# Kernel tuning notes

Hardware: AMD Instinct MI355X
Metric: run time of the kernel (lower is better)

The kernel has to match this reference:

```python
import jax, jax.numpy as jnp
import numpy as np

B = 256      # batch
ZD = 128     # z_dim
HIN = 128    # H_inputs
H = 512      # hidden
HT = 32      # H_t
N = 16384    # num nodes
RW = 16      # rw_len
TEMP = 1.0
P_DROP = 0.2
EPS_C = 0.1  # constraints epsilon


def setup_inputs() -> dict:
    key = jax.random.key(0)
    ks = jax.random.split(key, 20)
    def w(k, shape, fan):
        return (jax.random.normal(k, shape, jnp.float32) / np.float32(np.sqrt(fan)))
    z = lambda n: jnp.zeros((n,), jnp.float32)
    u = jax.random.uniform(ks[14], (RW, B, N), jnp.float32)
    return {
        "latent": jax.random.normal(ks[0], (B, ZD + 1), jnp.float32),
        "inputs0": jnp.zeros((B, HIN), jnp.float32),
        "Wc": w(ks[1], (ZD, ZD + 1), ZD + 1), "bc": z(ZD),
        "Ws": w(ks[2], (H, ZD), ZD), "bs": z(H),
        "Wh": w(ks[3], (H, H), H), "bh": z(H),
        "Wcc": w(ks[4], (H, H), H), "bcc": z(H),
        "W_ih": w(ks[5], (4 * H, HIN), HIN), "b_ih": z(4 * H),
        "W_hh": w(ks[6], (4 * H, H), H), "b_hh": z(4 * H),
        "W_up": w(ks[7], (N, H), H), "b_up": z(N),
        "W_down": w(ks[8], (HIN, N), N),
        "Wt_down": w(ks[9], (HT, H), H), "bt_down": z(HT),
        "Wt_pred": w(ks[10], (1, HT), HT),
        "Wt_up": w(ks[11], (HT, 1), 1), "bt_up": z(HT),
        "W_vt": w(ks[12], (HIN, HIN + HT), HIN + HT),
        "W_prob": w(ks[13], (1, HIN), HIN),
        # pre-sampled Gumbel noise per step (torch.rand -> gumbel)
        "gumbel": -jnp.log(-jnp.log(u + 1e-20) + 1e-20),
        # uniforms for dropout masks in TimeDecoder (forced train mode)
        "drop_u": jax.random.uniform(ks[15], (RW, B, HT), jnp.float32),
    }


def reference(latent, inputs0, Wc, bc, Ws, bs, Wh, bh, Wcc, bcc,
              W_ih, b_ih, W_hh, b_hh, W_up, b_up, W_down,
              Wt_down, bt_down, Wt_pred, Wt_up, bt_up, W_vt, W_prob,
              gumbel, drop_u):
    # induced=True path: compress latent, init (h, c)
    lat = jnp.tanh(latent @ Wc.T + bc)               # [B, ZD]
    s = jnp.tanh(lat @ Ws.T + bs)                    # [B, H]
    h0 = jnp.tanh(s @ Wh.T + bh)
    c0 = jnp.tanh(s @ Wcc.T + bcc)
    keep = 1.0 - P_DROP

    def step(carry, xs):
        x, h, c, last_t = carry
        g, du = xs
        # torch LSTMCell: gate order i, f, g, o
        gates = x @ W_ih.T + b_ih + h @ W_hh.T + b_hh  # [B, 4H]
        i, f, gg, o = jnp.split(gates, 4, axis=1)
        c2 = jax.nn.sigmoid(f) * c + jax.nn.sigmoid(i) * jnp.tanh(gg)
        h2 = jax.nn.sigmoid(o) * jnp.tanh(c2)
        # node logits + gumbel-softmax sample
        p = h2 @ W_up.T + b_up                         # [B, N]
        v = jax.nn.softmax((p + g) / TEMP, axis=1)
        Hg = v @ W_down.T                              # [B, HIN]
        # TimeDecoder (dropout always in train mode)
        td = jnp.tanh(h2 @ Wt_down.T + bt_down)        # [B, HT]
        td = td * (du < keep).astype(td.dtype) / keep
        t = jnp.minimum(td @ Wt_pred.T, 1.0)           # [B, 1]
        # constraints(t, last_t)
        mn = jnp.min(t)
        t = jnp.where(mn < EPS_C, t - mn, t)
        mx = jnp.max(t)
        t = jnp.where(mx > 1.0, t / mx, t)
        t = jnp.clip(t, last_t, 1.0)
        Ht = t @ Wt_up.T + bt_up                       # [B, HT]
        x2 = jnp.concatenate([Hg, Ht], axis=1) @ W_vt.T  # [B, HIN]
        return (x2, h2, c2, t), (v, t)

    last_t0 = jnp.zeros((latent.shape[0], 1), latent.dtype)
    (xf, _, _, _), (rw, ts) = jax.lax.scan(step, (inputs0, h0, c0, last_t0), (gumbel, drop_u))
    rw = jnp.transpose(rw, (1, 0, 2))   # [B, RW, N]
    ts = jnp.transpose(ts, (1, 0, 2))   # [B, RW, 1]
    prob = xf @ W_prob.T                # [B, 1]
    return rw, ts, prob
```

## Files before the change

kernel.cpp:

```cpp
#include <hip/hip_runtime.h>

typedef float  __attribute__((ext_vector_type(4))) f32x4;
typedef int    __attribute__((ext_vector_type(4))) i32x4;
typedef unsigned short u16;
typedef unsigned long long u64;

#define B    256
#define H    512
#define HIN  128
#define N    16384
#define RW   16
#define HT   32
#define KC2  672
#define RWN  262144
#define TS_OFF   67108864
#define PROB_OFF 67112960

__device__ __forceinline__ u16 f2bf(float f) {
  unsigned u = __builtin_bit_cast(unsigned, f);
  u += 0x7FFFu + ((u >> 16) & 1u);
  return (u16)(u >> 16);
}
__device__ __forceinline__ float bf2f(u16 v) {
  return __builtin_bit_cast(float, ((unsigned)v) << 16);
}
__device__ __forceinline__ float sigm(float x) { return 1.0f / (1.0f + expf(-x)); }

__device__ __forceinline__ void mfma(f32x4& d, i32x4 a, i32x4 b) {
  asm volatile("v_mfma_f32_16x16x32_bf16 %0, %1, %2, %0" : "+v"(d) : "v"(a), "v"(b));
}
__device__ __forceinline__ void mfma_n(f32x4& d, i32x4 a, i32x4 b) {
  asm volatile("s_nop 1\n\tv_mfma_f32_16x16x32_bf16 %0, %1, %2, %0" : "+v"(d) : "v"(a), "v"(b));
}
__device__ __forceinline__ void fence_acc(f32x4& v) {
  asm volatile("s_nop 7\n\ts_nop 7" : "+v"(v));
}

__global__ __launch_bounds__(256) void k_prep(
    const float* __restrict__ W_up, const float* __restrict__ W_down,
    const float* __restrict__ W_hh, const float* __restrict__ Wt_down,
    const float* __restrict__ b_ih, const float* __restrict__ b_hh,
    const float* __restrict__ Wh, const float* __restrict__ Wcc,
    const float* __restrict__ W_ih, const float* __restrict__ W_vt,
    const float* __restrict__ inputs0, const float* __restrict__ W_prob,
    u16* __restrict__ Wup_b, u16* __restrict__ Wdn_b, u16* __restrict__ Wfull,
    u16* __restrict__ Wtd_b, u16* __restrict__ Whc_b,
    float* __restrict__ bcomb, float* __restrict__ tstep, float* __restrict__ rowLs,
    float* __restrict__ g0add, float* __restrict__ wpc)
{
  const int idx0 = blockIdx.x * 256 + threadIdx.x;
  const int stride = gridDim.x * 256;
  for (int i = idx0; i < N * H; i += stride) Wup_b[i] = f2bf(W_up[i]);
  for (int i = idx0; i < HIN * N; i += stride) Wdn_b[i] = f2bf(W_down[i]);
  for (int i = idx0; i < 4 * H * H; i += stride) {
    int j = i >> 9, k = i & 511;
    Wfull[j * KC2 + 160 + k] = f2bf(W_hh[i]);
  }
  for (int i = idx0; i < HT * H; i += stride) Wtd_b[i] = f2bf(Wt_down[i]);
  for (int i = idx0; i < 2 * H * H; i += stride) {
    int j = i >> 9, k = i & 511;
    Whc_b[i] = f2bf(j < H ? Wh[j * H + k] : Wcc[(j - H) * H + k]);
  }
  for (int i = idx0; i < 4 * H; i += stride) bcomb[i] = b_ih[i] + b_hh[i];
  for (int i = idx0; i < B; i += stride) tstep[i] = 0.0f;
  for (int i = idx0; i < 16 * B; i += stride) rowLs[i] = 0.0f;
  for (int i = idx0; i < 2048 * 160; i += stride) {
    int j = i / 160, m = i - j * 160;
    float a = 0.0f;
    for (int c = 0; c < HIN; ++c) a += W_ih[j * HIN + c] * W_vt[c * 160 + m];
    Wfull[j * KC2 + m] = f2bf(a);
  }
  for (int i = idx0; i < 256 * 2048; i += stride) {
    int b = i >> 11, j = i & 2047;
    float a = 0.0f;
    for (int k = 0; k < HIN; ++k) a += inputs0[b * HIN + k] * W_ih[j * HIN + k];
    g0add[i] = a;
  }
  for (int i = idx0; i < 160; i += stride) {
    float a = 0.0f;
    for (int k = 0; k < HIN; ++k) a += W_prob[k] * W_vt[k * 160 + i];
    wpc[i] = a;
  }
}

__global__ __launch_bounds__(256) void k_lat(
    const float* __restrict__ latent, const float* __restrict__ Wc,
    const float* __restrict__ bc, float* __restrict__ latbuf)
{
  int idx = blockIdx.x * 256 + threadIdx.x;
  int b = idx >> 7, i = idx & 127;
  float acc = bc[i];
  for (int k = 0; k < 129; ++k) acc += latent[b * 129 + k] * Wc[i * 129 + k];
  latbuf[idx] = tanhf(acc);
}

__global__ __launch_bounds__(256) void k_sinit(
    const float* __restrict__ latbuf, const float* __restrict__ Ws,
    const float* __restrict__ bs, u16* __restrict__ sinit_b)
{
  int idx = blockIdx.x * 256 + threadIdx.x;
  int b = idx >> 9, j = idx & 511;
  float acc = bs[j];
  for (int k = 0; k < HIN; ++k) acc += latbuf[b * HIN + k] * Ws[j * HIN + k];
  sinit_b[idx] = f2bf(tanhf(acc));
}

__global__ __launch_bounds__(256) void k_h0c0m(
    const u16* __restrict__ sinit_b, const u16* __restrict__ Whc_b,
    const float* __restrict__ bh, const float* __restrict__ bcc,
    float* __restrict__ cbuf, u16* __restrict__ h0out)
{
  const int rb = blockIdx.x >> 6, cb = blockIdx.x & 63;
  const int wave = threadIdx.x >> 6, lane = threadIdx.x & 63;
  const int lr = lane & 15, lk = lane >> 4;
  const int m0 = rb * 16, col0 = cb * 16;
  const u16* ab = sinit_b + (m0 + lr) * H + wave * 128 + 8 * lk;
  const u16* bb = Whc_b + (col0 + lr) * H + wave * 128 + 8 * lk;
  f32x4 acc[2] = {};
  mfma_n(acc[0], *(const i32x4*)(ab),      *(const i32x4*)(bb));
  mfma_n(acc[1], *(const i32x4*)(ab + 32), *(const i32x4*)(bb + 32));
  mfma(acc[0], *(const i32x4*)(ab + 64), *(const i32x4*)(bb + 64));
  mfma(acc[1], *(const i32x4*)(ab + 96), *(const i32x4*)(bb + 96));
  fence_acc(acc[0]); fence_acc(acc[1]);
  __shared__ float q[4][16][17];
  #pragma unroll
  for (int rr = 0; rr < 4; ++rr)
    q[wave][4 * lk + rr][lr] = acc[0][rr] + acc[1][rr];
  __syncthreads();
  const int r2 = threadIdx.x >> 4, jj = threadIdx.x & 15;
  float s = q[0][r2][jj] + q[1][r2][jj] + q[2][r2][jj] + q[3][r2][jj];
  int col = col0 + jj;
  if (col < H) h0out[(m0 + r2) * H + col] = f2bf(tanhf(s + bh[col]));
  else         cbuf[(m0 + r2) * H + col - H] = tanhf(s + bcc[col - H]);
}

__global__ __launch_bounds__(256) void k_lstm2(
    const u16* __restrict__ hprev, u16* __restrict__ hcur,
    const u16* __restrict__ Wfull, const float* __restrict__ bcomb,
    float* __restrict__ cbuf, const float* __restrict__ g0,
    const float* __restrict__ HgXprev, float* __restrict__ HgXcur,
    const float* __restrict__ rowLs, const float* __restrict__ t0buf,
    float* __restrict__ tstep, const float* __restrict__ Wt_up,
    const float* __restrict__ bt_up, float* __restrict__ out, int r)
{
  const int blk = blockIdx.x, tid = threadIdx.x;
  const int wave = tid >> 6, lane = tid & 63;
  const int lr = lane & 15, lk = lane >> 4;
  const int rb = blk & 15, cb = blk >> 4;
  const int m0 = rb * 16, j0 = cb * 16;
  const float* rowLprev = rowLs + (r - 1) * B;

  __shared__ u16 aT[16][168];
  __shared__ float q[4][16][17];
  __shared__ float redS[8];
  __shared__ float tl[256];

  HgXcur[blk * 512 + tid] = 0.0f;
  HgXcur[blk * 512 + 256 + tid] = 0.0f;

  float tv = 0.0f;
  if (r > 0) {
    tv = t0buf[tid];
    float v = tv;
    #pragma unroll
    for (int off = 1; off < 64; off <<= 1) v = fminf(v, __shfl_xor(v, off));
    if (lane == 0) redS[wave] = v;
  }
  __syncthreads();
  if (r > 0) {
    float mn = fminf(fminf(redS[0], redS[1]), fminf(redS[2], redS[3]));
    if (mn < 0.1f) tv -= mn;
    float v = tv;
    #pragma unroll
    for (int off = 1; off < 64; off <<= 1) v = fmaxf(v, __shfl_xor(v, off));
    if (lane == 0) redS[4 + wave] = v;
  }
  __syncthreads();
  if (r > 0) {
    float mx = fmaxf(fmaxf(redS[4], redS[5]), fmaxf(redS[6], redS[7]));
    if (mx > 1.0f) tv /= mx;
    tv = fminf(fmaxf(tv, tstep[(r - 1) * B + tid]), 1.0f);
    if (blk == 0) {
      tstep[r * B + tid] = tv;
      out[TS_OFF + tid * RW + (r - 1)] = tv;
    }
  }
  tl[tid] = tv;

  {
    const int row = tid >> 4, c8 = (tid & 15) * 8;
    if (r > 0) {
      const float* hp = HgXprev + (size_t)(m0 + row) * HIN + c8;
      f32x4 A0 = {}, A1 = {};
      #pragma unroll
      for (int x = 0; x < 8; ++x) {
        A0 += *(const f32x4*)(hp + (size_t)x * (B * HIN));
        A1 += *(const f32x4*)(hp + (size_t)x * (B * HIN) + 4);
      }
      float R = 1.0f / rowLprev[m0 + row];
      aT[row][c8 + 0] = f2bf(A0[0] * R); aT[row][c8 + 1] = f2bf(A0[1] * R);
      aT[row][c8 + 2] = f2bf(A0[2] * R); aT[row][c8 + 3] = f2bf(A0[3] * R);
      aT[row][c8 + 4] = f2bf(A1[0] * R); aT[row][c8 + 5] = f2bf(A1[1] * R);
      aT[row][c8 + 6] = f2bf(A1[2] * R); aT[row][c8 + 7] = f2bf(A1[3] * R);
    } else {
      #pragma unroll
      for (int e = 0; e < 8; ++e) aT[row][c8 + e] = 0;
    }
  }
  __syncthreads();

  for (int i2 = tid; i2 < 512; i2 += 256) {
    int row = i2 >> 5, j = i2 & 31;
    aT[row][128 + j] = (r > 0) ? f2bf(tl[m0 + row] * Wt_up[j] + bt_up[j]) : (u16)0;
  }
  __syncthreads();

  const int gcol = wave * H + j0 + lr;
  f32x4 acc[2] = {};
  const u16* brow = Wfull + (size_t)gcol * KC2 + 8 * lk;
  const u16* aL   = &aT[lr][8 * lk];
  const u16* arow = hprev + (m0 + lr) * H + 8 * lk;
  mfma_n(acc[0], *(const i32x4*)(aL),       *(const i32x4*)(brow));
  mfma_n(acc[1], *(const i32x4*)(aL + 32),  *(const i32x4*)(brow + 32));
  mfma(acc[0], *(const i32x4*)(aL + 64),  *(const i32x4*)(brow + 64));
  mfma(acc[1], *(const i32x4*)(aL + 96),  *(const i32x4*)(brow + 96));
  mfma(acc[0], *(const i32x4*)(aL + 128), *(const i32x4*)(brow + 128));
  #pragma unroll 4
  for (int i = 5; i < 21; ++i) {
    int kk = i * 32;
    mfma(acc[i & 1], *(const i32x4*)(arow + kk - 160), *(const i32x4*)(brow + kk));
  }
  fence_acc(acc[0]); fence_acc(acc[1]);
  float bias = bcomb[gcol];
  #pragma unroll
  for (int rr = 0; rr < 4; ++rr)
    q[wave][4 * lk + rr][lr] = acc[0][rr] + acc[1][rr] + bias;
  __syncthreads();
  const int r2 = tid >> 4, jj = tid & 15;
  const int b = m0 + r2, j = j0 + jj;
  float gi = q[0][r2][jj], gf = q[1][r2][jj], gg = q[2][r2][jj], go = q[3][r2][jj];
  if (r == 0) {
    const float* gp = g0 + b * 2048 + j;
    gi += gp[0]; gf += gp[512]; gg += gp[1024]; go += gp[1536];
  }
  float c  = cbuf[b * H + j];
  float c2 = sigm(gf) * c + sigm(gi) * tanhf(gg);
  float h2 = sigm(go) * tanhf(c2);
  cbuf[b * H + j] = c2;
  hcur[b * H + j] = f2bf(h2);
}

__global__ __launch_bounds__(256) void k_pgemm2(
    const u16* __restrict__ hb, const u16* __restrict__ Wup,
    const float* __restrict__ b_up, const float* __restrict__ gum,
    u16* __restrict__ eb, const u16* __restrict__ ebp,
    float* __restrict__ rowL, const float* __restrict__ rowLs,
    float* __restrict__ HgX, const u16* __restrict__ Wdn,
    const u16* __restrict__ Wtd, const float* __restrict__ bt_down,
    const float* __restrict__ Wt_pred, const float* __restrict__ du,
    float* __restrict__ t0, float* __restrict__ out, int r)
{
  const int blk = blockIdx.x;
  const int rb = blk >> 7, cb = blk & 127;
  const int wave = threadIdx.x >> 6, lane = threadIdx.x & 63;
  const int lr = lane & 15, lk = lane >> 4;
  const int m0 = rb * 32;
  const int n0 = cb * 128 + wave * 32;

  float gv[2][4][2], bup0 = b_up[n0 + lr], bup1 = b_up[n0 + 16 + lr];
  #pragma unroll
  for (int mi = 0; mi < 2; ++mi)
    #pragma unroll
    for (int rr = 0; rr < 4; ++rr) {
      int row = m0 + 16 * mi + 4 * lk + rr;
      gv[mi][rr][0] = gum[(size_t)row * N + n0 + lr];
      gv[mi][rr][1] = gum[(size_t)row * N + n0 + 16 + lr];
    }

  if (r > 0) {
    const float* rowLprev = rowLs + (r - 1) * B;
    #pragma unroll
    for (int uu = 0; uu < 4; ++uu) {
      int flat = (blk * 1024 + uu * 256 + (int)threadIdx.x) * 4;
      int row = flat >> 14;
      float Rv = 1.0f / rowLprev[row];
      u64 ev = *(const u64*)(ebp + flat);
      f32x4 o;
      o[0] = bf2f((u16)ev) * Rv;
      o[1] = bf2f((u16)(ev >> 16)) * Rv;
      o[2] = bf2f((u16)(ev >> 32)) * Rv;
      o[3] = bf2f((u16)(ev >> 48)) * Rv;
      *(f32x4*)(out + (size_t)row * RWN + (size_t)(r - 1) * N + (flat & (N - 1))) = o;
    }
  }

  f32x4 acc[2][2] = {};
  const u16* a0 = hb + (m0 + lr) * H + 8 * lk;
  const u16* a1 = a0 + 16 * H;
  const u16* b0 = Wup + (size_t)(n0 + lr) * H + 8 * lk;
  const u16* b1 = b0 + 16 * H;
  {
    i32x4 af0 = *(const i32x4*)(a0);
    i32x4 af1 = *(const i32x4*)(a1);
    i32x4 bf0 = *(const i32x4*)(b0);
    i32x4 bf1 = *(const i32x4*)(b1);
    mfma_n(acc[0][0], af0, bf0); mfma_n(acc[0][1], af0, bf1);
    mfma_n(acc[1][0], af1, bf0); mfma_n(acc[1][1], af1, bf1);
  }
  #pragma unroll 3
  for (int kk = 32; kk < H; kk += 32) {
    i32x4 af0 = *(const i32x4*)(a0 + kk);
    i32x4 af1 = *(const i32x4*)(a1 + kk);
    i32x4 bf0 = *(const i32x4*)(b0 + kk);
    i32x4 bf1 = *(const i32x4*)(b1 + kk);
    mfma(acc[0][0], af0, bf0); mfma(acc[0][1], af0, bf1);
    mfma(acc[1][0], af1, bf0); mfma(acc[1][1], af1, bf1);
  }
  #pragma unroll
  for (int mi = 0; mi < 2; ++mi) { fence_acc(acc[mi][0]); fence_acc(acc[mi][1]); }

  __shared__ u16 eLb[32][136];
  __shared__ float sL[4][32];
  #pragma unroll
  for (int mi = 0; mi < 2; ++mi)
    #pragma unroll
    for (int rr = 0; rr < 4; ++rr) {
      int rl = 16 * mi + 4 * lk + rr;
      int row = m0 + rl;
      u16* sp = eb + (size_t)row * N + n0 + lr;
      float v0 = acc[mi][0][rr] + bup0 + gv[mi][rr][0];
      float v1 = acc[mi][1][rr] + bup1 + gv[mi][rr][1];
      float e0 = expf(fminf(v0, 80.0f));
      float e1 = expf(fminf(v1, 80.0f));
      u16 p0 = f2bf(e0), p1 = f2bf(e1);
      sp[0] = p0; sp[16] = p1;
      eLb[rl][wave * 32 + lr] = p0;
      eLb[rl][wave * 32 + 16 + lr] = p1;
      float par = e0 + e1;
      #pragma unroll
      for (int off = 1; off < 16; off <<= 1) par += __shfl_xor(par, off);
      if (lr == 0) sL[wave][rl] = par;
    }
  __syncthreads();
  if (threadIdx.x < 32)
    atomicAdd(rowL + m0 + threadIdx.x,
              sL[0][threadIdx.x] + sL[1][threadIdx.x] + sL[2][threadIdx.x] + sL[3][threadIdx.x]);

  const int nb = cb * 128;
  float* hgs = HgX + (size_t)(blk & 7) * (B * HIN);
  f32x4 acc2[2][2] = {};
  #pragma unroll
  for (int kk2 = 0; kk2 < 4; ++kk2) {
    i32x4 af0 = *(const i32x4*)(&eLb[lr][kk2 * 32 + 8 * lk]);
    i32x4 af1 = *(const i32x4*)(&eLb[16 + lr][kk2 * 32 + 8 * lk]);
    i32x4 bf0 = *(const i32x4*)(Wdn + (size_t)(wave * 32 + lr) * N + nb + kk2 * 32 + 8 * lk);
    i32x4 bf1 = *(const i32x4*)(Wdn + (size_t)(wave * 32 + 16 + lr) * N + nb + kk2 * 32 + 8 * lk);
    mfma(acc2[0][0], af0, bf0); mfma(acc2[0][1], af0, bf1);
    mfma(acc2[1][0], af1, bf0); mfma(acc2[1][1], af1, bf1);
  }
  #pragma unroll
  for (int mi2 = 0; mi2 < 2; ++mi2) { fence_acc(acc2[mi2][0]); fence_acc(acc2[mi2][1]); }
  #pragma unroll
  for (int mi2 = 0; mi2 < 2; ++mi2)
    #pragma unroll
    for (int ni = 0; ni < 2; ++ni)
      #pragma unroll
      for (int rr = 0; rr < 4; ++rr)
        atomicAdd(hgs + (m0 + 16 * mi2 + 4 * lk + rr) * HIN + wave * 32 + 16 * ni + lr,
                  acc2[mi2][ni][rr]);

  if (cb == 0 && wave < 2) {
    f32x4 acc3[2] = {};
    const u16* at = hb + (m0 + wave * 16 + lr) * H + 8 * lk;
    {
      i32x4 af = *(const i32x4*)(at);
      mfma_n(acc3[0], af, *(const i32x4*)(Wtd + lr * H + 8 * lk));
      mfma_n(acc3[1], af, *(const i32x4*)(Wtd + (16 + lr) * H + 8 * lk));
    }
    for (int kk = 32; kk < H; kk += 32) {
      i32x4 af = *(const i32x4*)(at + kk);
      mfma(acc3[0], af, *(const i32x4*)(Wtd + lr * H + kk + 8 * lk));
      mfma(acc3[1], af, *(const i32x4*)(Wtd + (16 + lr) * H + kk + 8 * lk));
    }
    fence_acc(acc3[0]); fence_acc(acc3[1]);
    float wp0 = Wt_pred[lr],  wp1 = Wt_pred[16 + lr];
    float bt0 = bt_down[lr],  bt1 = bt_down[16 + lr];
    #pragma unroll
    for (int rr = 0; rr < 4; ++rr) {
      int row = m0 + wave * 16 + 4 * lk + rr;
      float td0 = tanhf(acc3[0][rr] + bt0);
      float td1 = tanhf(acc3[1][rr] + bt1);
      td0 = (du[row * HT + lr]      < 0.8f) ? td0 * 1.25f : 0.0f;
      td1 = (du[row * HT + 16 + lr] < 0.8f) ? td1 * 1.25f : 0.0f;
      float part = td0 * wp0 + td1 * wp1;
      #pragma unroll
      for (int off = 1; off < 16; off <<= 1) part += __shfl_xor(part, off);
      if (lr == 0) t0[row] = fminf(part, 1.0f);
    }
  }
}

__global__ __launch_bounds__(256) void k_tail(
    float* __restrict__ out, const u16* __restrict__ eb15,
    const float* __restrict__ rowLs, const float* __restrict__ t0buf,
    float* __restrict__ tstep, const float* __restrict__ HgX15,
    const float* __restrict__ Wt_up, const float* __restrict__ bt_up,
    const float* __restrict__ wpc)
{
  const int blk = blockIdx.x, tid = threadIdx.x;
  const float* rowL15 = rowLs + 15 * B;
  if (blk < 1024) {
    #pragma unroll
    for (int uu = 0; uu < 4; ++uu) {
      int flat = (blk * 1024 + uu * 256 + tid) * 4;
      int row = flat >> 14;
      float Rv = 1.0f / rowL15[row];
      u64 ev = *(const u64*)(eb15 + flat);
      f32x4 o;
      o[0] = bf2f((u16)ev) * Rv;
      o[1] = bf2f((u16)(ev >> 16)) * Rv;
      o[2] = bf2f((u16)(ev >> 32)) * Rv;
      o[3] = bf2f((u16)(ev >> 48)) * Rv;
      *(f32x4*)(out + (size_t)row * RWN + (size_t)15 * N + (flat & (N - 1))) = o;
    }
  }
  if (blk == 0 || blk == 1024) {
    const int wave = tid >> 6, lane = tid & 63;
    __shared__ float redS[8];
    float tv = t0buf[tid];
    float v = tv;
    #pragma unroll
    for (int off = 1; off < 64; off <<= 1) v = fminf(v, __shfl_xor(v, off));
    if (lane == 0) redS[wave] = v;
    __syncthreads();
    float mn = fminf(fminf(redS[0], redS[1]), fminf(redS[2], redS[3]));
    if (mn < 0.1f) tv -= mn;
    v = tv;
    #pragma unroll
    for (int off = 1; off < 64; off <<= 1) v = fmaxf(v, __shfl_xor(v, off));
    if (lane == 0) redS[4 + wave] = v;
    __syncthreads();
    float mx = fmaxf(fmaxf(redS[4], redS[5]), fmaxf(redS[6], redS[7]));
    if (mx > 1.0f) tv /= mx;
    tv = fminf(fmaxf(tv, tstep[15 * B + tid]), 1.0f);
    if (blk == 0) out[TS_OFF + tid * RW + 15] = tv;
    else {
      float R = 1.0f / rowL15[tid];
      float acc = 0.0f;
      for (int m = 0; m < HIN; ++m) {
        float hg = 0.0f;
        #pragma unroll
        for (int x = 0; x < 8; ++x) hg += HgX15[(size_t)x * (B * HIN) + tid * HIN + m];
        acc += hg * R * wpc[m];
      }
      for (int j = 0; j < HT; ++j) acc += (tv * Wt_up[j] + bt_up[j]) * wpc[HIN + j];
      out[PROB_OFF + tid] = acc;
    }
  }
}

extern "C" void kernel_launch(void* const* d_in, const int* in_sizes, int n_in,
                              void* d_out, int out_size, void* d_ws, size_t ws_size,
                              hipStream_t stream) {
  (void)in_sizes; (void)n_in; (void)out_size; (void)ws_size;
  const float* latent  = (const float*)d_in[0];
  const float* inputs0 = (const float*)d_in[1];
  const float* Wc      = (const float*)d_in[2];
  const float* bc      = (const float*)d_in[3];
  const float* Ws      = (const float*)d_in[4];
  const float* bs      = (const float*)d_in[5];
  const float* Wh      = (const float*)d_in[6];
  const float* bh      = (const float*)d_in[7];
  const float* Wcc     = (const float*)d_in[8];
  const float* bcc     = (const float*)d_in[9];
  const float* W_ih    = (const float*)d_in[10];
  const float* b_ih    = (const float*)d_in[11];
  const float* W_hh    = (const float*)d_in[12];
  const float* b_hh    = (const float*)d_in[13];
  const float* W_up    = (const float*)d_in[14];
  const float* b_up    = (const float*)d_in[15];
  const float* W_down  = (const float*)d_in[16];
  const float* Wt_down = (const float*)d_in[17];
  const float* bt_down = (const float*)d_in[18];
  const float* Wt_pred = (const float*)d_in[19];
  const float* Wt_up   = (const float*)d_in[20];
  const float* bt_up   = (const float*)d_in[21];
  const float* W_vt    = (const float*)d_in[22];
  const float* W_prob  = (const float*)d_in[23];
  const float* gumbel  = (const float*)d_in[24];
  const float* drop_u  = (const float*)d_in[25];
  float* out = (float*)d_out;

  char* p = (char*)d_ws;
  auto alloc = [&](size_t bytes) { char* r = p; p += (bytes + 255) & ~(size_t)255; return r; };
  u16*   Wup_b  = (u16*)  alloc((size_t)N * H * 2);
  u16*   Wdn_b  = (u16*)  alloc((size_t)HIN * N * 2);
  u16*   Wfull_b= (u16*)  alloc((size_t)4 * H * KC2 * 2);
  u16*   Wtd_b  = (u16*)  alloc((size_t)HT * H * 2);
  u16*   Whc_b  = (u16*)  alloc((size_t)2 * H * H * 2);
  float* bcomb  = (float*)alloc(4 * H * 4);
  u16*   hbuf0  = (u16*)  alloc((size_t)B * H * 2);
  u16*   hbuf1  = (u16*)  alloc((size_t)B * H * 2);
  float* cbuf   = (float*)alloc((size_t)B * H * 4);
  u16*   sinit_b= (u16*)  alloc((size_t)B * H * 2);
  float* latbuf = (float*)alloc((size_t)B * HIN * 4);
  float* rowLs  = (float*)alloc((size_t)16 * B * 4);
  float* t0buf  = (float*)alloc(B * 4);
  float* tstep  = (float*)alloc((size_t)17 * B * 4);
  float* HgX0   = (float*)alloc((size_t)8 * B * HIN * 4);
  float* HgX1   = (float*)alloc((size_t)8 * B * HIN * 4);
  float* g0add  = (float*)alloc((size_t)B * 4 * H * 4);
  float* wpc    = (float*)alloc(160 * 4);
  u16*   ebuf0  = (u16*)  alloc((size_t)B * N * 2);
  u16*   ebuf1  = (u16*)  alloc((size_t)B * N * 2);

  k_prep<<<2048, 256, 0, stream>>>(W_up, W_down, W_hh, Wt_down, b_ih, b_hh, Wh, Wcc,
                                   W_ih, W_vt, inputs0, W_prob,
                                   Wup_b, Wdn_b, Wfull_b, Wtd_b, Whc_b, bcomb,
                                   tstep, rowLs, g0add, wpc);
  k_lat  <<<128, 256, 0, stream>>>(latent, Wc, bc, latbuf);
  k_sinit<<<512, 256, 0, stream>>>(latbuf, Ws, bs, sinit_b);
  k_h0c0m<<<1024, 256, 0, stream>>>(sinit_b, Whc_b, bh, bcc, cbuf, hbuf1);

  for (int r = 0; r < 16; ++r) {
    u16* hprev = (r & 1) ? hbuf0 : hbuf1;
    u16* hcur  = (r & 1) ? hbuf1 : hbuf0;
    u16* eb    = (r & 1) ? ebuf1 : ebuf0;
    u16* ebp   = (r & 1) ? ebuf0 : ebuf1;
    float* HgXc = (r & 1) ? HgX1 : HgX0;
    float* HgXp = (r & 1) ? HgX0 : HgX1;
    k_lstm2<<<512, 256, 0, stream>>>(hprev, hcur, Wfull_b, bcomb, cbuf, g0add,
                                     HgXp, HgXc, rowLs, t0buf, tstep,
                                     Wt_up, bt_up, out, r);
    k_pgemm2<<<1024, 256, 0, stream>>>(hcur, Wup_b, b_up, gumbel + (size_t)r * B * N,
                                       eb, ebp, rowLs + r * B, rowLs, HgXc, Wdn_b,
                                       Wtd_b, bt_down, Wt_pred,
                                       drop_u + (size_t)r * B * HT, t0buf, out, r);
  }
  k_tail<<<1025, 256, 0, stream>>>(out, ebuf1, rowLs, t0buf, tstep, HgX1,
                                   Wt_up, bt_up, wpc);
}
```

Baseline: 1.354 ms.

## Move recurrent h·W_hh GEMM into pgemm kernel and defer softmax normalization

The h@W_hh gate GEMM for the next step now runs inside k_pgemm2 and is stored in a gatesH buffer, so k_lstm2 for steps after the first only handles the small Hg/Ht part plus the gate math. Per-step normalize-and-write of the previous step's softmax output is removed. Unnormalized bf16 exponentials for all 16 steps are kept in one large buffer and normalized by a single final k_norm kernel. The eight sharded Hg atomic-accumulation buffers are merged into one. That removes the 8-way reduction read, but it raises atomic contention and needs more workspace.

```diff
diff --git a/kernel.cpp b/kernel.cpp
--- a/kernel.cpp
+++ b/kernel.cpp
@@ -135,10 +135,11 @@
 }
 
 __global__ __launch_bounds__(256) void k_lstm2(
-    const u16* __restrict__ hprev, u16* __restrict__ hcur,
+    const u16* __restrict__ h0buf, u16* __restrict__ hcur,
     const u16* __restrict__ Wfull, const float* __restrict__ bcomb,
     float* __restrict__ cbuf, const float* __restrict__ g0,
-    const float* __restrict__ HgXprev, float* __restrict__ HgXcur,
+    const float* __restrict__ gatesH,
+    const float* __restrict__ HgfPrev, float* __restrict__ HgfNext,
     const float* __restrict__ rowLs, const float* __restrict__ t0buf,
     float* __restrict__ tstep, const float* __restrict__ Wt_up,
     const float* __restrict__ bt_up, float* __restrict__ out, int r)
@@ -155,8 +156,7 @@
   __shared__ float redS[8];
   __shared__ float tl[256];
 
-  HgXcur[blk * 512 + tid] = 0.0f;
-  HgXcur[blk * 512 + 256 + tid] = 0.0f;
+  if (blk < 128) HgfNext[blk * 256 + tid] = 0.0f;
 
   float tv = 0.0f;
   if (r > 0) {
@@ -190,18 +190,14 @@
   {
     const int row = tid >> 4, c8 = (tid & 15) * 8;
     if (r > 0) {
-      const float* hp = HgXprev + (size_t)(m0 + row) * HIN + c8;
-      f32x4 A0 = {}, A1 = {};
-      #pragma unroll
-      for (int x = 0; x < 8; ++x) {
-        A0 += *(const f32x4*)(hp + (size_t)x * (B * HIN));
-        A1 += *(const f32x4*)(hp + (size_t)x * (B * HIN) + 4);
-      }
+      const float* hp = HgfPrev + (m0 + row) * HIN + c8;
+      f32x4 x0 = *(const f32x4*)hp;
+      f32x4 x1 = *(const f32x4*)(hp + 4);
       float R = 1.0f / rowLprev[m0 + row];
-      aT[row][c8 + 0] = f2bf(A0[0] * R); aT[row][c8 + 1] = f2bf(A0[1] * R);
-      aT[row][c8 + 2] = f2bf(A0[2] * R); aT[row][c8 + 3] = f2bf(A0[3] * R);
-      aT[row][c8 + 4] = f2bf(A1[0] * R); aT[row][c8 + 5] = f2bf(A1[1] * R);
-      aT[row][c8 + 6] = f2bf(A1[2] * R); aT[row][c8 + 7] = f2bf(A1[3] * R);
+      aT[row][c8 + 0] = f2bf(x0[0] * R); aT[row][c8 + 1] = f2bf(x0[1] * R);
+      aT[row][c8 + 2] = f2bf(x0[2] * R); aT[row][c8 + 3] = f2bf(x0[3] * R);
+      aT[row][c8 + 4] = f2bf(x1[0] * R); aT[row][c8 + 5] = f2bf(x1[1] * R);
+      aT[row][c8 + 6] = f2bf(x1[2] * R); aT[row][c8 + 7] = f2bf(x1[3] * R);
     } else {
       #pragma unroll
       for (int e = 0; e < 8; ++e) aT[row][c8 + e] = 0;
@@ -219,16 +215,18 @@
   f32x4 acc[2] = {};
   const u16* brow = Wfull + (size_t)gcol * KC2 + 8 * lk;
   const u16* aL   = &aT[lr][8 * lk];
-  const u16* arow = hprev + (m0 + lr) * H + 8 * lk;
   mfma_n(acc[0], *(const i32x4*)(aL),       *(const i32x4*)(brow));
   mfma_n(acc[1], *(const i32x4*)(aL + 32),  *(const i32x4*)(brow + 32));
   mfma(acc[0], *(const i32x4*)(aL + 64),  *(const i32x4*)(brow + 64));
   mfma(acc[1], *(const i32x4*)(aL + 96),  *(const i32x4*)(brow + 96));
   mfma(acc[0], *(const i32x4*)(aL + 128), *(const i32x4*)(brow + 128));
-  #pragma unroll 4
-  for (int i = 5; i < 21; ++i) {
-    int kk = i * 32;
-    mfma(acc[i & 1], *(const i32x4*)(arow + kk - 160), *(const i32x4*)(brow + kk));
+  if (r == 0) {
+    const u16* arow = h0buf + (m0 + lr) * H + 8 * lk;
+    #pragma unroll 4
+    for (int i = 5; i < 21; ++i) {
+      int kk = i * 32;
+      mfma(acc[i & 1], *(const i32x4*)(arow + kk - 160), *(const i32x4*)(brow + kk));
+    }
   }
   fence_acc(acc[0]); fence_acc(acc[1]);
   float bias = bcomb[gcol];
@@ -239,10 +237,8 @@
   const int r2 = tid >> 4, jj = tid & 15;
   const int b = m0 + r2, j = j0 + jj;
   float gi = q[0][r2][jj], gf = q[1][r2][jj], gg = q[2][r2][jj], go = q[3][r2][jj];
-  if (r == 0) {
-    const float* gp = g0 + b * 2048 + j;
-    gi += gp[0]; gf += gp[512]; gg += gp[1024]; go += gp[1536];
-  }
+  const float* gp = (r == 0) ? (g0 + b * 2048 + j) : (gatesH + b * 2048 + j);
+  gi += gp[0]; gf += gp[512]; gg += gp[1024]; go += gp[1536];
   float c  = cbuf[b * H + j];
   float c2 = sigm(gf) * c + sigm(gi) * tanhf(gg);
   float h2 = sigm(go) * tanhf(c2);
@@ -253,15 +249,14 @@
 __global__ __launch_bounds__(256) void k_pgemm2(
     const u16* __restrict__ hb, const u16* __restrict__ Wup,
     const float* __restrict__ b_up, const float* __restrict__ gum,
-    u16* __restrict__ eb, const u16* __restrict__ ebp,
-    float* __restrict__ rowL, const float* __restrict__ rowLs,
-    float* __restrict__ HgX, const u16* __restrict__ Wdn,
+    u16* __restrict__ ebufs, float* __restrict__ rowL,
+    float* __restrict__ HgfAcc, const u16* __restrict__ Wdn,
+    const u16* __restrict__ Wfull, float* __restrict__ gatesH,
     const u16* __restrict__ Wtd, const float* __restrict__ bt_down,
     const float* __restrict__ Wt_pred, const float* __restrict__ du,
-    float* __restrict__ t0, float* __restrict__ out, int r)
-{
-  const int blk = blockIdx.x;
-  const int rb = blk >> 7, cb = blk & 127;
+    float* __restrict__ t0, int r)
+{
+  const int rb = blockIdx.x >> 7, cb = blockIdx.x & 127;
   const int wave = threadIdx.x >> 6, lane = threadIdx.x & 63;
   const int lr = lane & 15, lk = lane >> 4;
   const int m0 = rb * 32;
@@ -276,23 +271,6 @@
       gv[mi][rr][0] = gum[(size_t)row * N + n0 + lr];
       gv[mi][rr][1] = gum[(size_t)row * N + n0 + 16 + lr];
     }
-
-  if (r > 0) {
-    const float* rowLprev = rowLs + (r - 1) * B;
-    #pragma unroll
-    for (int uu = 0; uu < 4; ++uu) {
-      int flat = (blk * 1024 + uu * 256 + (int)threadIdx.x) * 4;
-      int row = flat >> 14;
-      float Rv = 1.0f / rowLprev[row];
-      u64 ev = *(const u64*)(ebp + flat);
-      f32x4 o;
-      o[0] = bf2f((u16)ev) * Rv;
-      o[1] = bf2f((u16)(ev >> 16)) * Rv;
-      o[2] = bf2f((u16)(ev >> 32)) * Rv;
-      o[3] = bf2f((u16)(ev >> 48)) * Rv;
-      *(f32x4*)(out + (size_t)row * RWN + (size_t)(r - 1) * N + (flat & (N - 1))) = o;
-    }
-  }
 
   f32x4 acc[2][2] = {};
   const u16* a0 = hb + (m0 + lr) * H + 8 * lk;
@@ -321,13 +299,14 @@
 
   __shared__ u16 eLb[32][136];
   __shared__ float sL[4][32];
+  __shared__ float q2[2][16][17];
   #pragma unroll
   for (int mi = 0; mi < 2; ++mi)
     #pragma unroll
     for (int rr = 0; rr < 4; ++rr) {
       int rl = 16 * mi + 4 * lk + rr;
       int row = m0 + rl;
-      u16* sp = eb + (size_t)row * N + n0 + lr;
+      u16* sp = ebufs + (size_t)row * RWN + (size_t)r * N + n0 + lr;
       float v0 = acc[mi][0][rr] + bup0 + gv[mi][rr][0];
       float v1 = acc[mi][1][rr] + bup1 + gv[mi][rr][1];
       float e0 = expf(fminf(v0, 80.0f));
@@ -347,7 +326,6 @@
               sL[0][threadIdx.x] + sL[1][threadIdx.x] + sL[2][threadIdx.x] + sL[3][threadIdx.x]);
 
   const int nb = cb * 128;
-  float* hgs = HgX + (size_t)(blk & 7) * (B * HIN);
   f32x4 acc2[2][2] = {};
   #pragma unroll
   for (int kk2 = 0; kk2 < 4; ++kk2) {
@@ -366,8 +344,32 @@
     for (int ni = 0; ni < 2; ++ni)
       #pragma unroll
       for (int rr = 0; rr < 4; ++rr)
-        atomicAdd(hgs + (m0 + 16 * mi2 + 4 * lk + rr) * HIN + wave * 32 + 16 * ni + lr,
+        atomicAdd(HgfAcc + (m0 + 16 * mi2 + 4 * lk + rr) * HIN + wave * 32 + 16 * ni + lr,
                   acc2[mi2][ni][rr]);
+
+  {
+    const int rowtile = wave & 1, khalf = wave >> 1;
+    const int gc0 = cb * 16;
+    f32x4 acc4 = {};
+    const u16* ag = hb + (m0 + rowtile * 16 + lr) * H + khalf * 256 + 8 * lk;
+    const u16* bg = Wfull + (size_t)(gc0 + lr) * KC2 + 160 + khalf * 256 + 8 * lk;
+    mfma_n(acc4, *(const i32x4*)(ag), *(const i32x4*)(bg));
+    #pragma unroll
+    for (int kk = 32; kk < 256; kk += 32)
+      mfma(acc4, *(const i32x4*)(ag + kk), *(const i32x4*)(bg + kk));
+    fence_acc(acc4);
+    if (khalf == 1) {
+      #pragma unroll
+      for (int rr = 0; rr < 4; ++rr) q2[rowtile][4 * lk + rr][lr] = acc4[rr];
+    }
+    __syncthreads();
+    if (khalf == 0) {
+      #pragma unroll
+      for (int rr = 0; rr < 4; ++rr)
+        gatesH[(size_t)(m0 + rowtile * 16 + 4 * lk + rr) * 2048 + gc0 + lr] =
+            acc4[rr] + q2[rowtile][4 * lk + rr][lr];
+    }
+  }
 
   if (cb == 0 && wave < 2) {
     f32x4 acc3[2] = {};
@@ -400,31 +402,30 @@
   }
 }
 
-__global__ __launch_bounds__(256) void k_tail(
-    float* __restrict__ out, const u16* __restrict__ eb15,
+__global__ __launch_bounds__(256) void k_norm(
+    float* __restrict__ out, const u16* __restrict__ ebufs,
     const float* __restrict__ rowLs, const float* __restrict__ t0buf,
-    float* __restrict__ tstep, const float* __restrict__ HgX15,
+    const float* __restrict__ tstep, const float* __restrict__ Hgf15,
     const float* __restrict__ Wt_up, const float* __restrict__ bt_up,
     const float* __restrict__ wpc)
 {
   const int blk = blockIdx.x, tid = threadIdx.x;
-  const float* rowL15 = rowLs + 15 * B;
-  if (blk < 1024) {
-    #pragma unroll
-    for (int uu = 0; uu < 4; ++uu) {
-      int flat = (blk * 1024 + uu * 256 + tid) * 4;
-      int row = flat >> 14;
-      float Rv = 1.0f / rowL15[row];
-      u64 ev = *(const u64*)(eb15 + flat);
+  if (blk < 4096) {
+    #pragma unroll 4
+    for (int i = 0; i < 16; ++i) {
+      int flat4 = blk * 4096 + i * 256 + tid;
+      int base = flat4 * 4;
+      int b = base >> 18, r = (base >> 14) & 15;
+      float R = 1.0f / rowLs[r * B + b];
+      u64 ev = *(const u64*)(ebufs + base);
       f32x4 o;
-      o[0] = bf2f((u16)ev) * Rv;
-      o[1] = bf2f((u16)(ev >> 16)) * Rv;
-      o[2] = bf2f((u16)(ev >> 32)) * Rv;
-      o[3] = bf2f((u16)(ev >> 48)) * Rv;
-      *(f32x4*)(out + (size_t)row * RWN + (size_t)15 * N + (flat & (N - 1))) = o;
-    }
-  }
-  if (blk == 0 || blk == 1024) {
+      o[0] = bf2f((u16)ev) * R;
+      o[1] = bf2f((u16)(ev >> 16)) * R;
+      o[2] = bf2f((u16)(ev >> 32)) * R;
+      o[3] = bf2f((u16)(ev >> 48)) * R;
+      *(f32x4*)(out + base) = o;
+    }
+  } else {
     const int wave = tid >> 6, lane = tid & 63;
     __shared__ float redS[8];
     float tv = t0buf[tid];
@@ -443,19 +444,13 @@
     float mx = fmaxf(fmaxf(redS[4], redS[5]), fmaxf(redS[6], redS[7]));
     if (mx > 1.0f) tv /= mx;
     tv = fminf(fmaxf(tv, tstep[15 * B + tid]), 1.0f);
-    if (blk == 0) out[TS_OFF + tid * RW + 15] = tv;
-    else {
-      float R = 1.0f / rowL15[tid];
-      float acc = 0.0f;
-      for (int m = 0; m < HIN; ++m) {
-        float hg = 0.0f;
-        #pragma unroll
-        for (int x = 0; x < 8; ++x) hg += HgX15[(size_t)x * (B * HIN) + tid * HIN + m];
-        acc += hg * R * wpc[m];
-      }
-      for (int j = 0; j < HT; ++j) acc += (tv * Wt_up[j] + bt_up[j]) * wpc[HIN + j];
-      out[PROB_OFF + tid] = acc;
-    }
+    out[TS_OFF + tid * RW + 15] = tv;
+    float R = 1.0f / rowLs[15 * B + tid];
+    float acc = 0.0f;
+    for (int m = 0; m < HIN; ++m) acc += Hgf15[tid * HIN + m] * wpc[m];
+    acc *= R;
+    for (int j = 0; j < HT; ++j) acc += (tv * Wt_up[j] + bt_up[j]) * wpc[HIN + j];
+    out[PROB_OFF + tid] = acc;
   }
 }
 
@@ -501,18 +496,19 @@
   float* bcomb  = (float*)alloc(4 * H * 4);
   u16*   hbuf0  = (u16*)  alloc((size_t)B * H * 2);
   u16*   hbuf1  = (u16*)  alloc((size_t)B * H * 2);
+  u16*   h0buf  = (u16*)  alloc((size_t)B * H * 2);
   float* cbuf   = (float*)alloc((size_t)B * H * 4);
   u16*   sinit_b= (u16*)  alloc((size_t)B * H * 2);
   float* latbuf = (float*)alloc((size_t)B * HIN * 4);
   float* rowLs  = (float*)alloc((size_t)16 * B * 4);
   float* t0buf  = (float*)alloc(B * 4);
   float* tstep  = (float*)alloc((size_t)17 * B * 4);
-  float* HgX0   = (float*)alloc((size_t)8 * B * HIN * 4);
-  float* HgX1   = (float*)alloc((size_t)8 * B * HIN * 4);
+  float* Hgf2_0 = (float*)alloc((size_t)B * HIN * 4);
+  float* Hgf2_1 = (float*)alloc((size_t)B * HIN * 4);
   float* g0add  = (float*)alloc((size_t)B * 4 * H * 4);
+  float* gatesH = (float*)alloc((size_t)B * 4 * H * 4);
   float* wpc    = (float*)alloc(160 * 4);
-  u16*   ebuf0  = (u16*)  alloc((size_t)B * N * 2);
-  u16*   ebuf1  = (u16*)  alloc((size_t)B * N * 2);
+  u16*   ebufs  = (u16*)  alloc((size_t)B * RW * N * 2);
 
   k_prep<<<2048, 256, 0, stream>>>(W_up, W_down, W_hh, Wt_down, b_ih, b_hh, Wh, Wcc,
                                    W_ih, W_vt, inputs0, W_prob,
@@ -520,23 +516,21 @@
                                    tstep, rowLs, g0add, wpc);
   k_lat  <<<128, 256, 0, stream>>>(latent, Wc, bc, latbuf);
   k_sinit<<<512, 256, 0, stream>>>(latbuf, Ws, bs, sinit_b);
-  k_h0c0m<<<1024, 256, 0, stream>>>(sinit_b, Whc_b, bh, bcc, cbuf, hbuf1);
+  k_h0c0m<<<1024, 256, 0, stream>>>(sinit_b, Whc_b, bh, bcc, cbuf, h0buf);
 
   for (int r = 0; r < 16; ++r) {
-    u16* hprev = (r & 1) ? hbuf0 : hbuf1;
     u16* hcur  = (r & 1) ? hbuf1 : hbuf0;
-    u16* eb    = (r & 1) ? ebuf1 : ebuf0;
-    u16* ebp   = (r & 1) ? ebuf0 : ebuf1;
-    float* HgXc = (r & 1) ? HgX1 : HgX0;
-    float* HgXp = (r & 1) ? HgX0 : HgX1;
-    k_lstm2<<<512, 256, 0, stream>>>(hprev, hcur, Wfull_b, bcomb, cbuf, g0add,
-                                     HgXp, HgXc, rowLs, t0buf, tstep,
+    float* HgfCur  = (r & 1) ? Hgf2_1 : Hgf2_0;
+    float* HgfPrev = (r & 1) ? Hgf2_0 : Hgf2_1;
+    k_lstm2<<<512, 256, 0, stream>>>(h0buf, hcur, Wfull_b, bcomb, cbuf, g0add, gatesH,
+                                     HgfPrev, HgfCur, rowLs, t0buf, tstep,
                                      Wt_up, bt_up, out, r);
     k_pgemm2<<<1024, 256, 0, stream>>>(hcur, Wup_b, b_up, gumbel + (size_t)r * B * N,
-                                       eb, ebp, rowLs + r * B, rowLs, HgXc, Wdn_b,
+                                       ebufs, rowLs + r * B, HgfCur, Wdn_b,
+                                       Wfull_b, gatesH,
                                        Wtd_b, bt_down, Wt_pred,
-                                       drop_u + (size_t)r * B * HT, t0buf, out, r);
-  }
-  k_tail<<<1025, 256, 0, stream>>>(out, ebuf1, rowLs, t0buf, tstep, HgX1,
+                                       drop_u + (size_t)r * B * HT, t0buf, r);
+  }
+  k_norm<<<4097, 256, 0, stream>>>(out, ebufs, rowLs, t0buf, tstep, Hgf2_1,
                                    Wt_up, bt_up, wpc);
 }
```

Result: faster. 1.325 ms (-2.2%).
